# Kernel optimization log

Hardware: AMD Instinct MI355X
Metric: run time of the kernel (lower is better)

## Reference

```python
import jax, jax.numpy as jnp
import numpy as np

B, S, E, H, D = 4, 2048, 1024, 16, 64  # batch, seq (n_query==graph_size), embed, heads, qkv_dim


def setup_inputs() -> dict:
    key = jax.random.key(0)
    k1, k2, k3, k4, k5, k6 = jax.random.split(key, 6)
    q = jax.random.normal(k1, (B, S, E), dtype=jnp.float32)
    h = jax.random.normal(k2, (B, S, E), dtype=jnp.float32)
    # mask==True means attention NOT allowed (negative adjacency)
    mask = jax.random.randint(k3, (B, S, S), 0, 2) == 1
    scale = 0.02
    Wq = jax.random.normal(k4, (H * D, E), dtype=jnp.float32) * scale
    Wk = jax.random.normal(k5, (H * D, E), dtype=jnp.float32) * scale
    Wv = jax.random.normal(k6, (H * D, E), dtype=jnp.float32) * scale
    return {"q": q, "h": h, "mask": mask, "Wq": Wq, "Wk": Wk, "Wv": Wv}


def reference(q, h, mask, Wq, Wk, Wv):
    b, sq, e = q.shape
    sk = h.shape[1]
    hd = Wq.shape[0]
    heads = H
    d = hd // heads
    norm = 1.0 / jnp.sqrt(jnp.asarray(d, dtype=q.dtype))
    # Linear(bias=False): y = x @ W^T ; then reshape_by_heads -> (B, H, S, D)
    Q = (q @ Wq.T).reshape(b, sq, heads, d).transpose(0, 2, 1, 3)
    K = (h @ Wk.T).reshape(b, sk, heads, d).transpose(0, 2, 1, 3)
    V = (h @ Wv.T).reshape(b, sk, heads, d).transpose(0, 2, 1, 3)
    compat = norm * jnp.einsum("bhqd,bhkd->bhqk", Q, K)  # (B,H,Sq,Sk)
    compat = jnp.where(mask[:, None, :, :], -jnp.inf, compat)
    attn = jax.nn.softmax(compat, axis=-1)
    out_heads = jnp.einsum("bhqk,bhkd->bhqd", attn, V)
    # transpose(1,2) then concat heads -> (B, Sq, H*D)
    return out_heads.transpose(0, 2, 1, 3).reshape(b, sq, heads * d)
```

## Files before the change

### kernel.cpp

```cpp
#include <hip/hip_runtime.h>
#include <math.h>

#define Bb 4
#define Ss 2048
#define Ee 1024
#define Hh 16
#define Dd 64
#define HD (Hh * Dd)

typedef __attribute__((ext_vector_type(8))) _Float16 f16x8;
typedef __attribute__((ext_vector_type(4))) _Float16 f16x4;
typedef __attribute__((ext_vector_type(2))) _Float16 f16x2;
typedef __attribute__((ext_vector_type(4))) float f32x4;

__device__ __forceinline__ void gl_lds16(const void* g, void* l) {
  __builtin_amdgcn_global_load_lds(
      (const __attribute__((address_space(1))) unsigned int*)g,
      (__attribute__((address_space(3))) unsigned int*)l, 16, 0, 0);
}

__device__ __forceinline__ f16x2 pkrtz(float a, float b) {
  return __builtin_bit_cast(f16x2, __builtin_amdgcn_cvt_pkrtz(a, b));
}

#define CVT_BLOCKS 19456
__global__ __launch_bounds__(256) void prep_all(const float* __restrict__ q,
                                                const float* __restrict__ h,
                                                const float* __restrict__ wq,
                                                const float* __restrict__ wk,
                                                const float* __restrict__ wv,
                                                _Float16* __restrict__ qf,
                                                _Float16* __restrict__ hf,
                                                _Float16* __restrict__ wqf,
                                                _Float16* __restrict__ wkf,
                                                _Float16* __restrict__ wvf,
                                                const int* __restrict__ mask,
                                                unsigned long long* __restrict__ pm) {
  if (blockIdx.x < CVT_BLOCKS) {
    const int QH = (Bb * Ss * Ee) / 4;
    const int WM = (HD * Ee) / 4;
    int i = blockIdx.x * 256 + threadIdx.x;
    const float* src;
    _Float16* dst;
    int off;
    if (i < QH)                   { src = q;  dst = qf;  off = i; }
    else if (i < 2 * QH)          { src = h;  dst = hf;  off = i - QH; }
    else if (i < 2 * QH + WM)     { src = wq; dst = wqf; off = i - 2 * QH; }
    else if (i < 2 * QH + 2 * WM) { src = wk; dst = wkf; off = i - 2 * QH - WM; }
    else                          { src = wv; dst = wvf; off = i - 2 * QH - 2 * WM; }
    float4 v = ((const float4*)src)[off];
    f16x4 o;
    o.x = (_Float16)v.x; o.y = (_Float16)v.y;
    o.z = (_Float16)v.z; o.w = (_Float16)v.w;
    *(f16x4*)(dst + 4 * (size_t)off) = o;
  } else {
    const int bid = blockIdx.x - CVT_BLOCKS;
    const int wv = threadIdx.x >> 6, lane = threadIdx.x & 63;
    const size_t base = ((size_t)bid * 4 + wv) * 256;
#pragma unroll
    for (int i = 0; i < 4; ++i) {
      unsigned long long bits = __ballot(mask[base + i * 64 + lane] != 0);
      if (lane == 0) pm[(base >> 6) + i] = bits;
    }
  }
}

__global__ __launch_bounds__(512) void proj_qkv(const _Float16* __restrict__ qf,
                                                const _Float16* __restrict__ hf,
                                                const _Float16* __restrict__ Wqf,
                                                const _Float16* __restrict__ Wkf,
                                                const _Float16* __restrict__ Wvf,
                                                _Float16* __restrict__ Qb,
                                                _Float16* __restrict__ Kb,
                                                _Float16* __restrict__ Vb) {
  __shared__ _Float16 As[2][256 * 64];
  __shared__ _Float16 Bs[2][128 * 64];
  const int seg = blockIdx.y;
  const _Float16* A = (seg == 0) ? qf : hf;
  const _Float16* W = (seg == 0) ? Wqf : ((seg == 1) ? Wkf : Wvf);
  _Float16* Y       = (seg == 0) ? Qb  : ((seg == 1) ? Kb  : Vb);
  const float scale = (seg == 0) ? 0.18033688011112042f : 1.0f;

  const int lid = blockIdx.x;
  const int xcd = lid & 7, m = lid >> 3;
  const int stripe = xcd + 8 * (m & 3);
  const int nt = m >> 2;
  const int bm = stripe * 256, bn = nt * 128;

  const int tid = threadIdx.x;
  const int wv = tid >> 6, lane = tid & 63;
  const int quad = lane >> 4, l16 = lane & 15;
  const int wr = wv >> 1, wc = wv & 1;

  auto stage = [&](int buf, int k0) {
#pragma unroll
    for (int i = 0; i < 4; ++i) {
      int cb = wv * 64 + i * 512;
      int c = cb + lane;
      int row = c >> 3;
      int l = (c & 7) ^ (row & 7);
      gl_lds16(A + (size_t)(bm + row) * Ee + k0 + l * 8,
               (char*)&As[buf][0] + (size_t)cb * 16);
    }
#pragma unroll
    for (int i = 0; i < 2; ++i) {
      int cb = wv * 64 + i * 512;
      int c = cb + lane;
      int row = c >> 3;
      int l = (c & 7) ^ (row & 7);
      gl_lds16(W + (size_t)(bn + row) * Ee + k0 + l * 8,
               (char*)&Bs[buf][0] + (size_t)cb * 16);
    }
  };

  f32x4 acc[4][4];
#pragma unroll
  for (int i = 0; i < 4; ++i)
#pragma unroll
    for (int j = 0; j < 4; ++j) acc[i][j] = (f32x4){0.f, 0.f, 0.f, 0.f};

  stage(0, 0);
  const int NT = Ee / 64;
  for (int it = 0; it < NT; ++it) {
    const int buf = it & 1;
    if (it + 1 < NT) {
      stage(buf ^ 1, (it + 1) * 64);
      asm volatile("s_waitcnt vmcnt(6)\n\ts_barrier" ::: "memory");
    } else {
      asm volatile("s_waitcnt vmcnt(0)\n\ts_barrier" ::: "memory");
    }
#pragma unroll
    for (int s = 0; s < 2; ++s) {
      f16x8 af[4], bf[4];
#pragma unroll
      for (int i = 0; i < 4; ++i) {
        int row = wr * 64 + i * 16 + l16;
        int l = s * 4 + quad;
        af[i] = *(const f16x8*)&As[buf][row * 64 + ((l ^ (row & 7)) << 3)];
      }
#pragma unroll
      for (int j = 0; j < 4; ++j) {
        int row = wc * 64 + j * 16 + l16;
        int l = s * 4 + quad;
        bf[j] = *(const f16x8*)&Bs[buf][row * 64 + ((l ^ (row & 7)) << 3)];
      }
#pragma unroll
      for (int i = 0; i < 4; ++i)
#pragma unroll
        for (int j = 0; j < 4; ++j)
          acc[i][j] = __builtin_amdgcn_mfma_f32_16x16x32_f16(af[i], bf[j], acc[i][j], 0, 0, 0);
    }
    asm volatile("s_barrier" ::: "memory");
  }

#pragma unroll
  for (int i = 0; i < 4; ++i)
#pragma unroll
    for (int j = 0; j < 4; ++j)
#pragma unroll
      for (int reg = 0; reg < 4; ++reg) {
        int row = bm + wr * 64 + i * 16 + quad * 4 + reg;
        int col = bn + wc * 64 + j * 16 + l16;
        Y[(size_t)row * HD + col] = (_Float16)(acc[i][j][reg] * scale);
      }
}

__global__ __launch_bounds__(256) void vtrans(const unsigned short* __restrict__ Vb,
                                              unsigned short* __restrict__ Vt) {
  __shared__ unsigned short T[64][68];
  const int nx = blockIdx.x;
  const int my = blockIdx.y;
  const int m0 = my * 64, n0 = nx * 64;
  const int bsel = m0 >> 11, s0 = m0 & 2047;
  const int tid = threadIdx.x;
  const int r = tid >> 4, c4 = (tid & 15) << 2;
#pragma unroll
  for (int i = 0; i < 4; ++i) {
    ushort4 v = *(const ushort4*)(Vb + (size_t)(m0 + r + i * 16) * HD + n0 + c4);
    T[r + i * 16][c4 + 0] = v.x; T[r + i * 16][c4 + 1] = v.y;
    T[r + i * 16][c4 + 2] = v.z; T[r + i * 16][c4 + 3] = v.w;
  }
  __syncthreads();
#pragma unroll
  for (int i = 0; i < 4; ++i) {
    ushort4 o;
    o.x = T[c4 + 0][r + i * 16]; o.y = T[c4 + 1][r + i * 16];
    o.z = T[c4 + 2][r + i * 16]; o.w = T[c4 + 3][r + i * 16];
    *(ushort4*)(Vt + ((size_t)bsel * HD + n0 + r + i * 16) * Ss + s0 + c4) = o;
  }
}

__global__ __launch_bounds__(256) void attn_mfma5(const _Float16* __restrict__ Qb,
                                                  const _Float16* __restrict__ Kb,
                                                  const _Float16* __restrict__ Vt,
                                                  const unsigned long long* __restrict__ pm,
                                                  float* __restrict__ out) {
  const int bq = blockIdx.x;
  const int h  = blockIdx.y;
  const int b  = blockIdx.z;
  const int tid  = threadIdx.x;
  const int wv   = tid >> 6;
  const int lane = tid & 63;
  const int quad = lane >> 4;
  const int l16  = lane & 15;

  __shared__ _Float16 Ks[64][72];
  __shared__ _Float16 Vs[64][72];

  const int q0g = bq * 128 + wv * 32;
  f16x8 qf[2][2];
#pragma unroll
  for (int g = 0; g < 2; ++g) {
    const _Float16* qrow = Qb + ((size_t)b * Ss + q0g + g * 16 + l16) * HD + h * Dd;
    qf[g][0] = *(const f16x8*)(qrow + quad * 8);
    qf[g][1] = *(const f16x8*)(qrow + 32 + quad * 8);
  }

  const int r = tid >> 2, c = (tid & 3) << 4;
  const _Float16* kbase = Kb + ((size_t)b * Ss + r) * HD + h * Dd + c;
  const _Float16* vbase = Vt + (((size_t)b * Hh + h) * Dd + r) * Ss + c;

  const unsigned long long* pmrow0 = pm + ((size_t)b * Ss + q0g + l16) * (Ss >> 6);
  const size_t pmg = (size_t)16 * (Ss >> 6);

  f32x4 O[2][4];
#pragma unroll
  for (int g = 0; g < 2; ++g)
#pragma unroll
    for (int dt = 0; dt < 4; ++dt) O[g][dt] = (f32x4){0.f, 0.f, 0.f, 0.f};
  float lsum[2] = {0.f, 0.f};

  f16x8 ka = *(const f16x8*)kbase;
  f16x8 kb2 = *(const f16x8*)(kbase + 8);
  f16x8 va = *(const f16x8*)vbase;
  f16x8 vb2 = *(const f16x8*)(vbase + 8);

  for (int kt = 0; kt < Ss; kt += 64) {
    __syncthreads();
    *(f16x8*)&Ks[r][c]     = ka;
    *(f16x8*)&Ks[r][c + 8] = kb2;
    *(f16x8*)&Vs[r][c]     = va;
    *(f16x8*)&Vs[r][c + 8] = vb2;
    {
      const int ktn = (kt + 64) & (Ss - 1);
      ka  = *(const f16x8*)(kbase + (size_t)ktn * HD);
      kb2 = *(const f16x8*)(kbase + (size_t)ktn * HD + 8);
      va  = *(const f16x8*)(vbase + ktn);
      vb2 = *(const f16x8*)(vbase + ktn + 8);
    }
    asm volatile("s_waitcnt lgkmcnt(0)\n\ts_barrier" ::: "memory");

    f32x4 c4[2][4];
#pragma unroll
    for (int g = 0; g < 2; ++g)
#pragma unroll
      for (int sub = 0; sub < 4; ++sub) c4[g][sub] = (f32x4){0.f, 0.f, 0.f, 0.f};
    __builtin_amdgcn_s_setprio(1);
#pragma unroll
    for (int sub = 0; sub < 4; ++sub) {
      f16x8 k0 = *(const f16x8*)&Ks[sub * 16 + l16][quad * 8];
      f16x8 k1 = *(const f16x8*)&Ks[sub * 16 + l16][32 + quad * 8];
#pragma unroll
      for (int g = 0; g < 2; ++g) {
        c4[g][sub] = __builtin_amdgcn_mfma_f32_16x16x32_f16(k0, qf[g][0], c4[g][sub], 0, 0, 0);
        c4[g][sub] = __builtin_amdgcn_mfma_f32_16x16x32_f16(k1, qf[g][1], c4[g][sub], 0, 0, 0);
      }
    }
    __builtin_amdgcn_s_setprio(0);

    f16x4 pf[2][4];
#pragma unroll
    for (int g = 0; g < 2; ++g) {
      const unsigned long long mq = pmrow0[(g ? pmg : 0) + (kt >> 6)] >> (quad * 4);
#pragma unroll
      for (int sub = 0; sub < 4; ++sub) {
        float p[4];
#pragma unroll
        for (int reg = 0; reg < 4; ++reg) {
          float t = ((mq >> (sub * 16 + reg)) & 1ull) ? -3.0e38f : c4[g][sub][reg];
          p[reg] = __builtin_amdgcn_exp2f(t);
          lsum[g] += p[reg];
        }
        f16x2 lo = pkrtz(p[0], p[1]);
        f16x2 hi = pkrtz(p[2], p[3]);
        pf[g][sub] = __builtin_shufflevector(lo, hi, 0, 1, 2, 3);
      }
    }

    __builtin_amdgcn_s_setprio(1);
#pragma unroll
    for (int dt = 0; dt < 4; ++dt)
#pragma unroll
      for (int sub = 0; sub < 4; ++sub) {
        f16x4 vf = *(const f16x4*)&Vs[dt * 16 + l16][sub * 16 + quad * 4];
#pragma unroll
        for (int g = 0; g < 2; ++g)
          O[g][dt] = __builtin_amdgcn_mfma_f32_16x16x16f16(vf, pf[g][sub], O[g][dt], 0, 0, 0);
      }
    __builtin_amdgcn_s_setprio(0);
  }

#pragma unroll
  for (int g = 0; g < 2; ++g) {
    float ls = lsum[g];
    ls += __shfl_xor(ls, 16, 64);
    ls += __shfl_xor(ls, 32, 64);
    const float inv = 1.0f / ls;
    float* obase = out + ((size_t)b * Ss + q0g + g * 16 + l16) * HD + h * Dd;
#pragma unroll
    for (int dt = 0; dt < 4; ++dt) {
      float4 st;
      st.x = O[g][dt][0] * inv; st.y = O[g][dt][1] * inv;
      st.z = O[g][dt][2] * inv; st.w = O[g][dt][3] * inv;
      *(float4*)(obase + dt * 16 + quad * 4) = st;
    }
  }
}

extern "C" void kernel_launch(void* const* d_in, const int* in_sizes, int n_in,
                              void* d_out, int out_size, void* d_ws, size_t ws_size,
                              hipStream_t stream) {
  const float* q    = (const float*)d_in[0];
  const float* h    = (const float*)d_in[1];
  const int*   mask = (const int*)d_in[2];
  const float* Wq   = (const float*)d_in[3];
  const float* Wk   = (const float*)d_in[4];
  const float* Wv   = (const float*)d_in[5];
  float* out = (float*)d_out;

  char* ws = (char*)d_ws;
  const size_t MB = 1024 * 1024;
  _Float16* qf  = (_Float16*)(ws);
  _Float16* hf  = (_Float16*)(ws + 16 * MB);
  _Float16* Wqf = (_Float16*)(ws + 32 * MB);
  _Float16* Wkf = (_Float16*)(ws + 34 * MB);
  _Float16* Wvf = (_Float16*)(ws + 36 * MB);
  _Float16* Qb  = (_Float16*)(ws + 38 * MB);
  _Float16* Kb  = (_Float16*)(ws + 54 * MB);
  _Float16* Vb  = (_Float16*)(ws + 70 * MB);
  _Float16* Vt  = (_Float16*)(ws);
  unsigned long long* pm = (unsigned long long*)(ws + 86 * MB);

  const int mask_blocks = (Bb * Ss * Ss) / 1024;
  prep_all<<<CVT_BLOCKS + mask_blocks, 256, 0, stream>>>(
      q, h, Wq, Wk, Wv, qf, hf, Wqf, Wkf, Wvf, mask, pm);

  proj_qkv<<<dim3(256, 3), 512, 0, stream>>>(qf, hf, Wqf, Wkf, Wvf, Qb, Kb, Vb);

  vtrans<<<dim3(HD / 64, (Bb * Ss) / 64), 256, 0, stream>>>((const unsigned short*)Vb,
                                                            (unsigned short*)Vt);

  attn_mfma5<<<dim3(Ss / 128, Hh, Bb), 256, 0, stream>>>(Qb, Kb, Vt, pm, out);
}
```

Before: 368.4 us.

## Swizzle K/V LDS tiles, prefetch mask words, use bitwise masking and fdot2 row sums

Removes the padding from the K and V shared-memory tiles and replaces it with an XOR swizzle, applied on both the writes and the MFMA operand reads, to avoid bank conflicts while using less LDS. Mask words are now loaded one iteration ahead alongside the K/V prefetch. Masking is done with an AND on the bits of exp2's result instead of a select before the exp. Row sums are accumulated from the packed fp16 values with fdot2. The risks are subtle indexing errors in the swizzle, and the row sum now uses fp16-rounded values, which matches what the PV MFMA consumes.

```diff
diff --git a/kernel.cpp b/kernel.cpp
--- a/kernel.cpp
+++ b/kernel.cpp
@@ -190,7 +190,7 @@
   }
 }
 
-__global__ __launch_bounds__(256) void attn_mfma5(const _Float16* __restrict__ Qb,
+__global__ __launch_bounds__(256) void attn_mfma6(const _Float16* __restrict__ Qb,
                                                   const _Float16* __restrict__ Kb,
                                                   const _Float16* __restrict__ Vt,
                                                   const unsigned long long* __restrict__ pm,
@@ -204,8 +204,8 @@
   const int quad = lane >> 4;
   const int l16  = lane & 15;
 
-  __shared__ _Float16 Ks[64][72];
-  __shared__ _Float16 Vs[64][72];
+  __shared__ _Float16 Ks[64][64];
+  __shared__ _Float16 Vs[64][64];
 
   const int q0g = bq * 128 + wv * 32;
   f16x8 qf[2][2];
@@ -217,6 +217,11 @@
   }
 
   const int r = tid >> 2, c = (tid & 3) << 4;
+  const int swzr = (r & 7) ^ ((r & 4) >> 2);
+  const int pw0 = ((c >> 3) ^ swzr) << 3;
+  const int pw1 = pw0 ^ 8;
+  const int swzl = (l16 & 7) ^ ((l16 & 4) >> 2);
+
   const _Float16* kbase = Kb + ((size_t)b * Ss + r) * HD + h * Dd + c;
   const _Float16* vbase = Vt + (((size_t)b * Hh + h) * Dd + r) * Ss + c;
 
@@ -229,24 +234,31 @@
 #pragma unroll
     for (int dt = 0; dt < 4; ++dt) O[g][dt] = (f32x4){0.f, 0.f, 0.f, 0.f};
   float lsum[2] = {0.f, 0.f};
+  const f16x2 one2 = {(_Float16)1.0f, (_Float16)1.0f};
 
   f16x8 ka = *(const f16x8*)kbase;
   f16x8 kb2 = *(const f16x8*)(kbase + 8);
   f16x8 va = *(const f16x8*)vbase;
   f16x8 vb2 = *(const f16x8*)(vbase + 8);
+  unsigned long long mqn0 = ~pmrow0[0];
+  unsigned long long mqn1 = ~pmrow0[pmg];
 
   for (int kt = 0; kt < Ss; kt += 64) {
-    __syncthreads();
-    *(f16x8*)&Ks[r][c]     = ka;
-    *(f16x8*)&Ks[r][c + 8] = kb2;
-    *(f16x8*)&Vs[r][c]     = va;
-    *(f16x8*)&Vs[r][c + 8] = vb2;
+    asm volatile("s_waitcnt lgkmcnt(0)\n\ts_barrier" ::: "memory");
+    *(f16x8*)&Ks[r][pw0] = ka;
+    *(f16x8*)&Ks[r][pw1] = kb2;
+    *(f16x8*)&Vs[r][pw0] = va;
+    *(f16x8*)&Vs[r][pw1] = vb2;
+    const unsigned long long mq0 = mqn0, mq1 = mqn1;
     {
       const int ktn = (kt + 64) & (Ss - 1);
       ka  = *(const f16x8*)(kbase + (size_t)ktn * HD);
       kb2 = *(const f16x8*)(kbase + (size_t)ktn * HD + 8);
       va  = *(const f16x8*)(vbase + ktn);
       vb2 = *(const f16x8*)(vbase + ktn + 8);
+      const int itn = (ktn >> 6);
+      mqn0 = ~pmrow0[itn];
+      mqn1 = ~pmrow0[pmg + itn];
     }
     asm volatile("s_waitcnt lgkmcnt(0)\n\ts_barrier" ::: "memory");
 
@@ -258,8 +270,10 @@
     __builtin_amdgcn_s_setprio(1);
 #pragma unroll
     for (int sub = 0; sub < 4; ++sub) {
-      f16x8 k0 = *(const f16x8*)&Ks[sub * 16 + l16][quad * 8];
-      f16x8 k1 = *(const f16x8*)&Ks[sub * 16 + l16][32 + quad * 8];
+      const _Float16* krow = &Ks[sub * 16 + l16][0];
+      const int off0 = (quad ^ swzl) << 3;
+      f16x8 k0 = *(const f16x8*)(krow + off0);
+      f16x8 k1 = *(const f16x8*)(krow + (off0 ^ 32));
 #pragma unroll
       for (int g = 0; g < 2; ++g) {
         c4[g][sub] = __builtin_amdgcn_mfma_f32_16x16x32_f16(k0, qf[g][0], c4[g][sub], 0, 0, 0);
@@ -271,32 +285,46 @@
     f16x4 pf[2][4];
 #pragma unroll
     for (int g = 0; g < 2; ++g) {
-      const unsigned long long mq = pmrow0[(g ? pmg : 0) + (kt >> 6)] >> (quad * 4);
+      const unsigned long long mqs = (g ? mq1 : mq0) >> (quad * 4);
+      const unsigned kw0 = (unsigned)mqs;
+      const unsigned kw1 = (unsigned)(mqs >> 32);
 #pragma unroll
       for (int sub = 0; sub < 4; ++sub) {
+        const unsigned word = (sub < 2) ? kw0 : kw1;
         float p[4];
 #pragma unroll
         for (int reg = 0; reg < 4; ++reg) {
-          float t = ((mq >> (sub * 16 + reg)) & 1ull) ? -3.0e38f : c4[g][sub][reg];
-          p[reg] = __builtin_amdgcn_exp2f(t);
-          lsum[g] += p[reg];
+          const int pos = (sub & 1) * 16 + reg;
+          const unsigned keep = (unsigned)(((int)(word << (31 - pos))) >> 31);
+          float e = __builtin_amdgcn_exp2f(c4[g][sub][reg]);
+          p[reg] = __builtin_bit_cast(float,
+                     __builtin_bit_cast(unsigned, e) & keep);
         }
         f16x2 lo = pkrtz(p[0], p[1]);
         f16x2 hi = pkrtz(p[2], p[3]);
+#if __has_builtin(__builtin_amdgcn_fdot2)
+        lsum[g] = __builtin_amdgcn_fdot2(lo, one2, lsum[g], false);
+        lsum[g] = __builtin_amdgcn_fdot2(hi, one2, lsum[g], false);
+#else
+        lsum[g] += (p[0] + p[1]) + (p[2] + p[3]);
+#endif
         pf[g][sub] = __builtin_shufflevector(lo, hi, 0, 1, 2, 3);
       }
     }
 
     __builtin_amdgcn_s_setprio(1);
 #pragma unroll
-    for (int dt = 0; dt < 4; ++dt)
+    for (int dt = 0; dt < 4; ++dt) {
+      const _Float16* vrow = &Vs[dt * 16 + l16][0];
 #pragma unroll
       for (int sub = 0; sub < 4; ++sub) {
-        f16x4 vf = *(const f16x4*)&Vs[dt * 16 + l16][sub * 16 + quad * 4];
+        f16x4 vf = *(const f16x4*)(vrow + ((((2 * sub + (quad >> 1)) ^ swzl) << 3) +
+                                           ((quad & 1) << 2)));
 #pragma unroll
         for (int g = 0; g < 2; ++g)
           O[g][dt] = __builtin_amdgcn_mfma_f32_16x16x16f16(vf, pf[g][sub], O[g][dt], 0, 0, 0);
       }
+    }
     __builtin_amdgcn_s_setprio(0);
   }
 
@@ -350,5 +378,5 @@
   vtrans<<<dim3(HD / 64, (Bb * Ss) / 64), 256, 0, stream>>>((const unsigned short*)Vb,
                                                             (unsigned short*)Vt);
 
-  attn_mfma5<<<dim3(Ss / 128, Hh, Bb), 256, 0, stream>>>(Qb, Kb, Vt, pm, out);
-}
+  attn_mfma6<<<dim3(Ss / 128, Hh, Bb), 256, 0, stream>>>(Qb, Kb, Vt, pm, out);
+}
```

Result: no change. 364.9 us (-0.9%).
